# Kernel tuning notes

Measured on AMD Instinct MI355X. Metric: run time of the kernel, lower is better.

The kernel has to match this reference:

```python
import jax, jax.numpy as jnp
import numpy as np

B, N, C = 8, 32768, 4
M = 11          # memory_length
D = 5           # degree
K = D * M       # basis size per (channel, time) = M linear + (D-1)*M envelope terms


def setup_inputs() -> dict:
    key = jax.random.key(0)
    kx, kw = jax.random.split(key)
    x = jax.random.normal(kx, (B, N, C, 2), dtype=jnp.float32)
    # xavier-uniform over [C, K]
    limit = float(np.sqrt(6.0 / (C + K)))
    Weight = jax.random.uniform(kw, (C, K), minval=-limit, maxval=limit, dtype=jnp.float32)
    return {"x": x, "Weight": Weight}


def _windows(a, m):
    # a: [..., L] -> [..., L-m+1, m]; windows[..., n, j] = a[..., n+j]
    n_out = a.shape[-1] - m + 1
    return jnp.stack([a[..., j:j + n_out] for j in range(m)], axis=-1)


def reference(x, Weight):
    b, n, c, _ = x.shape
    # [B,N,C,2] -> complex [B,C,N]
    xc = (x[..., 0] + 1j * x[..., 1]).transpose(0, 2, 1)
    pad = jnp.zeros((b, c, M - 1), dtype=xc.dtype)
    padded = jnp.concatenate([pad, xc], axis=2)                 # [B,C,N+M-1]
    windows_x = _windows(padded, M)                             # [B,C,N,M] complex
    amp = jnp.abs(padded)                                       # [B,C,N+M-1]
    x_degree = jnp.stack([amp ** i for i in range(1, D)], axis=1)  # [B,D-1,C,L]
    windows_degree = _windows(x_degree, M)                      # [B,D-1,C,N,M]
    mul_term = windows_x[:, None] * windows_degree              # [B,D-1,C,N,M] complex
    mul_term = mul_term.transpose(0, 2, 3, 1, 4).reshape(b, c, n, (D - 1) * M)
    x_input = jnp.concatenate([windows_x, mul_term], axis=3)    # [B,C,N,D*M]
    out_c = jnp.einsum('bcnk,ck->bcn', x_input, Weight.astype(x_input.dtype))
    out_c = out_c.transpose(0, 2, 1)                            # [B,N,C]
    return jnp.stack([out_c.real, out_c.imag], axis=3)          # [B,N,C,2]
```

## Files before the change

kernel.cpp:

```cpp
#include <hip/hip_runtime.h>

#define BB 8
#define NN 32768
#define CC 4
#define MM 11
#define KK 55
#define THREADS 256
#define HALO (MM - 1)
#define SS (THREADS + HALO)


__global__ __launch_bounds__(THREADS, 8)
void gmp_kernel(const float* __restrict__ x,
                const float* __restrict__ W,
                float* __restrict__ out) {
    __shared__ float4 zs[SS];
    __shared__ float2 as2[SS];

    const int tid = threadIdx.x;
    const int b  = blockIdx.y;
    const int h  = blockIdx.z;
    const int n0 = blockIdx.x * THREADS;

    const float4* xg = (const float4*)x + (size_t)b * NN * 2;

    for (int s = tid; s < SS; s += THREADS) {
        const int t = n0 - HALO + s;
        float4 v = make_float4(0.f, 0.f, 0.f, 0.f);
        if (t >= 0) v = xg[2 * t + h];
        float2 a;
        a.x = sqrtf(fmaf(v.x, v.x, v.y * v.y));
        a.y = sqrtf(fmaf(v.z, v.z, v.w * v.w));
        zs[s] = v;
        as2[s] = a;
    }
    __syncthreads();

    const float* W0 = W + (2 * h) * KK;
    const float* W1 = W + (2 * h + 1) * KK;

    float ar0 = 0.f, ai0 = 0.f, ar1 = 0.f, ai1 = 0.f;

    #pragma unroll
    for (int j = 0; j < MM; j++) {
        const int s = tid + j;
        const float4 v = zs[s];
        const float2 a = as2[s];
        {
            float p = W0[4 * MM + j];
            p = fmaf(p, a.x, W0[3 * MM + j]);
            p = fmaf(p, a.x, W0[2 * MM + j]);
            p = fmaf(p, a.x, W0[1 * MM + j]);
            p = fmaf(p, a.x, W0[0 * MM + j]);
            ar0 = fmaf(v.x, p, ar0);
            ai0 = fmaf(v.y, p, ai0);
        }
        {
            float p = W1[4 * MM + j];
            p = fmaf(p, a.y, W1[3 * MM + j]);
            p = fmaf(p, a.y, W1[2 * MM + j]);
            p = fmaf(p, a.y, W1[1 * MM + j]);
            p = fmaf(p, a.y, W1[0 * MM + j]);
            ar1 = fmaf(v.z, p, ar1);
            ai1 = fmaf(v.w, p, ai1);
        }
    }

    const int n = n0 + tid;
    float4* og = (float4*)out + ((size_t)(b * NN + n) * 2 + h);
    *og = make_float4(ar0, ai0, ar1, ai1);
}

extern "C" void kernel_launch(void* const* d_in, const int* in_sizes, int n_in,
                              void* d_out, int out_size, void* d_ws, size_t ws_size,
                              hipStream_t stream) {
    const float* x = (const float*)d_in[0];
    const float* W = (const float*)d_in[1];
    float* out = (float*)d_out;

    dim3 grid(NN / THREADS, BB, 2);
    gmp_kernel<<<grid, THREADS, 0, stream>>>(x, W, out);
}
```

Baseline: 63.28 us.

## Interleave channel-pair halves across threads for contiguous float4 loads

Each block now covers 128 samples with both channel-pair halves: consecutive threads handle the even and odd float4 of the same sample. The shared-memory staging loads a contiguous float4 range instead of every other float4, and the output store is fully contiguous. This removes the strided half-utilized global accesses of the previous grid split. It adds per-thread weight selection, which may cost uniform scalar weight loads, and the halo is reloaded more often because tiles are smaller.

```diff
diff --git a/kernel.cpp b/kernel.cpp
--- a/kernel.cpp
+++ b/kernel.cpp
@@ -6,68 +6,71 @@
 #define MM 11
 #define KK 55
 #define THREADS 256
+#define SAMP 128
 #define HALO (MM - 1)
-#define SS (THREADS + HALO)
+#define SS2 (SAMP + HALO)
+#define NF4 (2 * SS2)
 
+
+__device__ __forceinline__ float wsel(const float* __restrict__ Wrow, bool hi, int o) {
+    float lo = Wrow[o];
+    float hv = Wrow[2 * KK + o];
+    return hi ? hv : lo;
+}
 
 __global__ __launch_bounds__(THREADS, 8)
 void gmp_kernel(const float* __restrict__ x,
                 const float* __restrict__ W,
                 float* __restrict__ out) {
-    __shared__ float4 zs[SS];
-    __shared__ float2 as2[SS];
+    __shared__ float4 zs[NF4];
+    __shared__ float2 as2[NF4];
 
     const int tid = threadIdx.x;
     const int b  = blockIdx.y;
-    const int h  = blockIdx.z;
-    const int n0 = blockIdx.x * THREADS;
+    const int n0 = blockIdx.x * SAMP;
 
     const float4* xg = (const float4*)x + (size_t)b * NN * 2;
+    const int g0 = (n0 - HALO) * 2;
 
-    for (int s = tid; s < SS; s += THREADS) {
-        const int t = n0 - HALO + s;
+    for (int idx = tid; idx < NF4; idx += THREADS) {
         float4 v = make_float4(0.f, 0.f, 0.f, 0.f);
-        if (t >= 0) v = xg[2 * t + h];
-        float2 a;
-        a.x = sqrtf(fmaf(v.x, v.x, v.y * v.y));
-        a.y = sqrtf(fmaf(v.z, v.z, v.w * v.w));
-        zs[s] = v;
-        as2[s] = a;
+        if (g0 + idx >= 0) v = xg[g0 + idx];
+        zs[idx] = v;
+        as2[idx] = make_float2(sqrtf(fmaf(v.x, v.x, v.y * v.y)),
+                               sqrtf(fmaf(v.z, v.z, v.w * v.w)));
     }
     __syncthreads();
 
-    const float* W0 = W + (2 * h) * KK;
-    const float* W1 = W + (2 * h + 1) * KK;
+    const bool hi = (tid & 1);
 
     float ar0 = 0.f, ai0 = 0.f, ar1 = 0.f, ai1 = 0.f;
 
     #pragma unroll
     for (int j = 0; j < MM; j++) {
-        const int s = tid + j;
-        const float4 v = zs[s];
-        const float2 a = as2[s];
+        const float4 v = zs[tid + 2 * j];
+        const float2 a = as2[tid + 2 * j];
         {
-            float p = W0[4 * MM + j];
-            p = fmaf(p, a.x, W0[3 * MM + j]);
-            p = fmaf(p, a.x, W0[2 * MM + j]);
-            p = fmaf(p, a.x, W0[1 * MM + j]);
-            p = fmaf(p, a.x, W0[0 * MM + j]);
-            ar0 = fmaf(v.x, p, ar0);
-            ai0 = fmaf(v.y, p, ai0);
+            float pw = wsel(W, hi, 4 * MM + j);
+            pw = fmaf(pw, a.x, wsel(W, hi, 3 * MM + j));
+            pw = fmaf(pw, a.x, wsel(W, hi, 2 * MM + j));
+            pw = fmaf(pw, a.x, wsel(W, hi, 1 * MM + j));
+            pw = fmaf(pw, a.x, wsel(W, hi, 0 * MM + j));
+            ar0 = fmaf(v.x, pw, ar0);
+            ai0 = fmaf(v.y, pw, ai0);
         }
         {
-            float p = W1[4 * MM + j];
-            p = fmaf(p, a.y, W1[3 * MM + j]);
-            p = fmaf(p, a.y, W1[2 * MM + j]);
-            p = fmaf(p, a.y, W1[1 * MM + j]);
-            p = fmaf(p, a.y, W1[0 * MM + j]);
-            ar1 = fmaf(v.z, p, ar1);
-            ai1 = fmaf(v.w, p, ai1);
+            const float* W1 = W + KK;
+            float pw = wsel(W1, hi, 4 * MM + j);
+            pw = fmaf(pw, a.y, wsel(W1, hi, 3 * MM + j));
+            pw = fmaf(pw, a.y, wsel(W1, hi, 2 * MM + j));
+            pw = fmaf(pw, a.y, wsel(W1, hi, 1 * MM + j));
+            pw = fmaf(pw, a.y, wsel(W1, hi, 0 * MM + j));
+            ar1 = fmaf(v.z, pw, ar1);
+            ai1 = fmaf(v.w, pw, ai1);
         }
     }
 
-    const int n = n0 + tid;
-    float4* og = (float4*)out + ((size_t)(b * NN + n) * 2 + h);
+    float4* og = (float4*)out + ((size_t)(b * NN + n0) * 2 + tid);
     *og = make_float4(ar0, ai0, ar1, ai1);
 }
 
@@ -78,6 +81,6 @@
     const float* W = (const float*)d_in[1];
     float* out = (float*)d_out;
 
-    dim3 grid(NN / THREADS, BB, 2);
+    dim3 grid(NN / SAMP, BB, 1);
     gmp_kernel<<<grid, THREADS, 0, stream>>>(x, W, out);
 }
```

New measurement: 83.93 us. +32.6%, slower.
